# Kernel tuning notes

Measured on AMD Instinct MI355X. Metric: run time of the kernel, lower is better.

The kernel has to match this reference:

```python
import jax, jax.numpy as jnp
import numpy as np

B, CQ, CKV, E = 8, 256, 256, 256
H, W = 64, 64
HP, WP = 32, 32


def setup_inputs() -> dict:
    key = jax.random.key(0)
    ks = jax.random.split(key, 6)
    C = jax.random.normal(ks[0], (B, CQ, H, W), dtype=jnp.float32)
    P = jax.random.normal(ks[1], (B, CKV, HP, WP), dtype=jnp.float32)
    # 1x1 conv weights, kaiming-ish scale; stored as [out_ch, in_ch]
    theta_w = jax.random.normal(ks[2], (E, CQ), dtype=jnp.float32) * (1.0 / np.sqrt(CQ))
    phi_w = jax.random.normal(ks[3], (E, CKV), dtype=jnp.float32) * (1.0 / np.sqrt(CKV))
    g_w = jax.random.normal(ks[4], (E, CKV), dtype=jnp.float32) * (1.0 / np.sqrt(CKV))
    out_w = jax.random.normal(ks[5], (CQ, E), dtype=jnp.float32) * (1.0 / np.sqrt(E))
    return {"C": C, "P": P, "theta_w": theta_w, "phi_w": phi_w, "g_w": g_w, "out_w": out_w}


def reference(C, P, theta_w, phi_w, g_w, out_w):
    b, _, h, w = C.shape
    e = theta_w.shape[0]
    # 1x1 convs are channel GEMMs
    theta_C = jnp.einsum('bchw,ec->behw', C, theta_w).reshape(b, e, h * w)   # [B,E,Nq]
    phi_P = jnp.einsum('bchw,ec->behw', P, phi_w).reshape(b, e, -1)          # [B,E,Nkv]
    g_P = jnp.einsum('bchw,ec->behw', P, g_w).reshape(b, e, -1)              # [B,E,Nkv]
    attn = jnp.einsum('ben,bem->bnm', theta_C, phi_P) / (e ** 0.5)           # [B,Nq,Nkv]
    attn = jax.nn.softmax(attn, axis=-1)
    out = jnp.einsum('bem,bnm->ben', g_P, attn).reshape(b, e, h, w)          # [B,E,H,W]
    out = jnp.einsum('behw,ce->bchw', out, out_w)                            # [B,CQ,H,W]
    return jnp.concatenate([C, out], axis=1)
```

## Files before the change

### kernel.cpp

```cpp
#include <hip/hip_runtime.h>


typedef __attribute__((ext_vector_type(8))) short short8;
typedef __attribute__((ext_vector_type(16))) float f32x16;
typedef unsigned short ushort_t;

__device__ __forceinline__ unsigned short f2bf(float f) {
    unsigned int u = __float_as_uint(f);
    u += 0x7FFFu + ((u >> 16) & 1u);
    return (unsigned short)(u >> 16);
}
__device__ __forceinline__ unsigned int pack2bf(float a, float b) {
    return (unsigned int)f2bf(a) | ((unsigned int)f2bf(b) << 16);
}
__device__ __forceinline__ void gload16(const ushort_t* g, ushort_t* l) {
    __builtin_amdgcn_global_load_lds(
        (const __attribute__((address_space(1))) unsigned int*)g,
        (__attribute__((address_space(3))) unsigned int*)l, 16, 0, 0);
}
__device__ __forceinline__ f32x16 zero16() {
    f32x16 z;
#pragma unroll
    for (int i = 0; i < 16; ++i) z[i] = 0.f;
    return z;
}

__global__ __launch_bounds__(256) void prep_w(const float* __restrict__ thw,
                                              const float* __restrict__ phw,
                                              const float* __restrict__ ow,
                                              const float* __restrict__ gw,
                                              ushort_t* __restrict__ thc,
                                              ushort_t* __restrict__ phc,
                                              ushort_t* __restrict__ w2c) {
    int blk = blockIdx.x;
    int t = threadIdx.x;
    if (blk < 512) {
        int which = blk >> 8;
        int e = blk & 255, c = t;
        const float* src = which ? phw : thw;
        ushort_t* dst = which ? phc : thc;
        int idx = ((((e >> 5) * 16 + (c >> 4)) * 64 + ((c >> 3) & 1) * 32 + (e & 31)) << 3) + (c & 7);
        dst[idx] = f2bf(src[e * 256 + c]);
    } else {
        int c0 = (blk - 512) * 8;
        float acc[8] = {};
        for (int e = 0; e < 256; ++e) {
            float g = gw[e * 256 + t];
#pragma unroll
            for (int i = 0; i < 8; ++i) acc[i] += ow[(c0 + i) * 256 + e] * g;
        }
#pragma unroll
        for (int i = 0; i < 8; ++i) {
            int c = c0 + i, k = t;
            int idx = ((((c >> 5) * 16 + (k >> 4)) * 64 + ((k >> 3) & 1) * 32 + (c & 31)) << 3) + (k & 7);
            w2c[idx] = f2bf(acc[i]);
        }
    }
}

__global__ __launch_bounds__(256, 2) void proj_all(const ushort_t* __restrict__ thc,
                                                   const ushort_t* __restrict__ phc,
                                                   const ushort_t* __restrict__ w2c,
                                                   const float* __restrict__ C,
                                                   const float* __restrict__ P,
                                                   ushort_t* __restrict__ thetaA,
                                                   ushort_t* __restrict__ phiA,
                                                   ushort_t* __restrict__ gVx) {
    __shared__ float Xs[256][68];
    int blk = blockIdx.x;
    int tid = threadIdx.x, lane = tid & 63, wid = tid >> 6;
    int l31 = lane & 31, lh = lane >> 5;
    const int wq = wid & 1, we = wid >> 1;

    int role, b, nt, N;
    const ushort_t* Wc;
    const float* Xg;
    ushort_t* outp;
    float scale = 1.f;
    if (blk < 512) {
        role = 0; b = blk & 7; nt = blk >> 3;
        Wc = thc; Xg = C + (size_t)b * 1048576; outp = thetaA + (size_t)b * 1048576;
        N = 4096; scale = 1.4426950408889634f / 16.0f;
    } else if (blk < 640) {
        int r = blk - 512; role = 1; b = r & 7; nt = r >> 3;
        Wc = phc; Xg = P + (size_t)b * 262144; outp = phiA + (size_t)b * 262144;
        N = 1024;
    } else {
        int r = blk - 640; role = 2; b = r & 7; nt = r >> 3;
        Wc = w2c; Xg = P + (size_t)b * 262144; outp = gVx + (size_t)b * 262144;
        N = 1024;
    }

    {
        const float* Xb = Xg + nt * 64;
#pragma unroll
        for (int i = 0; i < 16; ++i) {
            int idx = i * 256 + tid;
            int row = idx >> 4, c4 = (idx & 15) * 4;
            *(float4*)&Xs[row][c4] = *(const float4*)(Xb + (size_t)row * N + c4);
        }
    }
    __syncthreads();

    const int n0 = nt * 64 + wq * 32;
    const int ncr = (n0 >> 5) * 16;
    const int q = wq * 32 + l31;

    f32x16 o[4];
#pragma unroll
    for (int f = 0; f < 4; ++f) o[f] = zero16();

#pragma unroll
    for (int ks = 0; ks < 16; ++ks) {
        const int cb = ks * 16 + lh * 8;
        union PW { unsigned int u[4]; short8 v; } xw;
#pragma unroll
        for (int j = 0; j < 4; ++j)
            xw.u[j] = pack2bf(Xs[cb + 2 * j][q], Xs[cb + 2 * j + 1][q]);
#pragma unroll
        for (int f2 = 0; f2 < 4; ++f2) {
            int f = we * 4 + f2;
            short8 wf = *(const short8*)(Wc + ((size_t)(f * 16 + ks) * 64 + lane) * 8);
            o[f2] = __builtin_amdgcn_mfma_f32_32x32x16_bf16(wf, xw.v, o[f2], 0, 0, 0);
        }
    }

    if (role < 2) {
#pragma unroll
        for (int f2 = 0; f2 < 4; ++f2) {
            int f = we * 4 + f2;
#pragma unroll
            for (int rq = 0; rq < 4; ++rq) {
                uint2 st;
                st.x = pack2bf(o[f2][4 * rq + 0] * scale, o[f2][4 * rq + 1] * scale);
                st.y = pack2bf(o[f2][4 * rq + 2] * scale, o[f2][4 * rq + 3] * scale);
                size_t addr = ((size_t)(ncr + f * 2 + (rq >> 1)) * 64 + l31 + 32 * (rq & 1)) * 8 + 4 * lh;
                *(uint2*)(outp + addr) = st;
            }
        }
    } else {
        int kvq = (n0 >> 4) + (l31 >> 4);
        int lhw = 32 * ((l31 >> 3) & 1);
        int kl = l31 & 7;
#pragma unroll
        for (int f2 = 0; f2 < 4; ++f2) {
            int f = we * 4 + f2;
#pragma unroll
            for (int r2 = 0; r2 < 16; ++r2) {
                int crow = (r2 & 3) + 8 * (r2 >> 2) + 4 * lh;
                size_t addr = ((size_t)(f * 64 + kvq) * 64 + crow + lhw) * 8 + kl;
                outp[addr] = f2bf(o[f2][r2]);
            }
        }
    }
}

__global__ __launch_bounds__(512, 2) void attn9(const ushort_t* __restrict__ thetaA,
                                                const ushort_t* __restrict__ phiA,
                                                const ushort_t* __restrict__ gVx,
                                                const float* __restrict__ Cf,
                                                float* __restrict__ out) {
    const int b = blockIdx.x & 7, qt = blockIdx.x >> 3;
    const int tid = threadIdx.x, lane = tid & 63, wid = tid >> 6;
    const int l31 = lane & 31, lh = lane >> 5;
    const int g = wid & 3, eh = wid >> 2;

    __shared__ __align__(16) ushort_t smem[65536];

    const ushort_t* thA = thetaA + (size_t)b * 1048576;
    const ushort_t* phA = phiA + (size_t)b * 262144;
    const ushort_t* gVb = gVx + (size_t)b * 262144;

    auto stage = [&](int j, int d) {
        if (wid < 4) {
            const ushort_t* src = phA + (size_t)j * 16384 + (size_t)wid * 4096 + lane * 8;
            ushort_t* dst = smem + d * 16384 + wid * 4096;
#pragma unroll
            for (int i = 0; i < 8; ++i) gload16(src + i * 512, dst + i * 512);
        } else {
            int w = wid - 4;
#pragma unroll
            for (int q2 = 0; q2 < 2; ++q2) {
                int f = w * 2 + q2;
#pragma unroll
                for (int jj = 0; jj < 4; ++jj) {
                    const ushort_t* src = gVb + ((size_t)(f * 64 + j * 4 + jj) * 64 + lane) * 8;
                    ushort_t* dst = smem + 32768 + d * 16384 + f * 2048 + jj * 512;
                    gload16(src, dst);
                }
            }
        }
    };

    stage(0, 0);

    short8 qf[16];
    {
        const int qcr = (qt * 4 + g) * 16;
#pragma unroll
        for (int ks = 0; ks < 16; ++ks)
            qf[ks] = *(const short8*)(thA + ((size_t)(qcr + ks) * 64 + lane) * 8);
    }

    f32x16 o[4];
#pragma unroll
    for (int f = 0; f < 4; ++f) o[f] = zero16();
    float rl = 0.f;

    const size_t cbase = (size_t)b * 1048576 + (size_t)qt * 128 + (size_t)l31 * 4;
    const size_t dofs = (size_t)b * 1048576;
    size_t cpo = 0;
    float4 cpv;

    for (int it = 0; it < 16; ++it) {
        asm volatile("s_waitcnt vmcnt(0)" ::: "memory");
        __builtin_amdgcn_s_barrier();
        __builtin_amdgcn_sched_barrier(0);
        if (it < 15) stage(it + 1, (it + 1) & 1);

        if (it > 0) *(float4*)(out + cpo + dofs) = cpv;
        cpo = cbase + (size_t)(it * 16 + 2 * wid + lh) * 4096;
        cpv = *(const float4*)(Cf + cpo);

        const ushort_t* Kb = smem + (it & 1) * 16384;
        const ushort_t* Vb = smem + 32768 + (it & 1) * 16384 + eh * 8192;

        f32x16 s0 = zero16(), s1 = zero16();
#pragma unroll
        for (int ks = 0; ks < 16; ++ks) {
            short8 kf0 = *(const short8*)(Kb + (size_t)ks * 512 + lane * 8);
            short8 kf1 = *(const short8*)(Kb + 8192 + (size_t)ks * 512 + lane * 8);
            s0 = __builtin_amdgcn_mfma_f32_32x32x16_bf16(kf0, qf[ks], s0, 0, 0, 0);
            s1 = __builtin_amdgcn_mfma_f32_32x32x16_bf16(kf1, qf[ks], s1, 0, 0, 0);
        }

        float ps = 0.f;
#pragma unroll
        for (int r = 0; r < 16; ++r) {
            s0[r] = __builtin_amdgcn_exp2f(s0[r]);
            s1[r] = __builtin_amdgcn_exp2f(s1[r]);
            ps += s0[r] + s1[r];
        }
        ps += __shfl_xor(ps, 32);
        rl += ps;

        unsigned int a0 = pack2bf(s0[0], s0[1]),   b0 = pack2bf(s0[4], s0[5]);
        unsigned int a1 = pack2bf(s0[2], s0[3]),   b1 = pack2bf(s0[6], s0[7]);
        unsigned int a2 = pack2bf(s0[8], s0[9]),   b2 = pack2bf(s0[12], s0[13]);
        unsigned int a3 = pack2bf(s0[10], s0[11]), b3 = pack2bf(s0[14], s0[15]);
        asm volatile("v_permlane32_swap_b32 %0, %1" : "+v"(a0), "+v"(b0));
        asm volatile("v_permlane32_swap_b32 %0, %1" : "+v"(a1), "+v"(b1));
        asm volatile("v_permlane32_swap_b32 %0, %1" : "+v"(a2), "+v"(b2));
        asm volatile("v_permlane32_swap_b32 %0, %1" : "+v"(a3), "+v"(b3));
        unsigned int c0 = pack2bf(s1[0], s1[1]),   d0 = pack2bf(s1[4], s1[5]);
        unsigned int c1 = pack2bf(s1[2], s1[3]),   d1 = pack2bf(s1[6], s1[7]);
        unsigned int c2 = pack2bf(s1[8], s1[9]),   d2 = pack2bf(s1[12], s1[13]);
        unsigned int c3 = pack2bf(s1[10], s1[11]), d3 = pack2bf(s1[14], s1[15]);
        asm volatile("v_permlane32_swap_b32 %0, %1" : "+v"(c0), "+v"(d0));
        asm volatile("v_permlane32_swap_b32 %0, %1" : "+v"(c1), "+v"(d1));
        asm volatile("v_permlane32_swap_b32 %0, %1" : "+v"(c2), "+v"(d2));
        asm volatile("v_permlane32_swap_b32 %0, %1" : "+v"(c3), "+v"(d3));
        union PW { unsigned int u[4]; short8 v; };
        PW pw[4];
        pw[0].u[0] = a0; pw[0].u[1] = a1; pw[0].u[2] = b0; pw[0].u[3] = b1;
        pw[1].u[0] = a2; pw[1].u[1] = a3; pw[1].u[2] = b2; pw[1].u[3] = b3;
        pw[2].u[0] = c0; pw[2].u[1] = c1; pw[2].u[2] = d0; pw[2].u[3] = d1;
        pw[3].u[0] = c2; pw[3].u[1] = c3; pw[3].u[2] = d2; pw[3].u[3] = d3;

        __builtin_amdgcn_s_setprio(1);
#pragma unroll
        for (int ks2 = 0; ks2 < 4; ++ks2) {
            short8 pf = pw[ks2].v;
#pragma unroll
            for (int fl = 0; fl < 4; ++fl) {
                short8 vf = *(const short8*)(Vb + (size_t)fl * 2048 + ks2 * 512 + lane * 8);
                o[fl] = __builtin_amdgcn_mfma_f32_32x32x16_bf16(vf, pf, o[fl], 0, 0, 0);
            }
        }
        __builtin_amdgcn_s_setprio(0);
    }

    *(float4*)(out + cpo + dofs) = cpv;

    float inv = 1.f / rl;
    float* ob = out + (size_t)b * 2097152 + (size_t)256 * 4096 + qt * 128 + g * 32 + l31;
#pragma unroll
    for (int fl = 0; fl < 4; ++fl) {
#pragma unroll
        for (int r = 0; r < 16; ++r) {
            int e = eh * 128 + fl * 32 + (r & 3) + 8 * (r >> 2) + 4 * lh;
            ob[(size_t)e * 4096] = o[fl][r] * inv;
        }
    }
}


extern "C" void kernel_launch(void* const* d_in, const int* in_sizes, int n_in,
                              void* d_out, int out_size, void* d_ws, size_t ws_size,
                              hipStream_t stream) {
    const float* C       = (const float*)d_in[0];
    const float* P       = (const float*)d_in[1];
    const float* theta_w = (const float*)d_in[2];
    const float* phi_w   = (const float*)d_in[3];
    const float* g_w     = (const float*)d_in[4];
    const float* out_w   = (const float*)d_in[5];
    float* out = (float*)d_out;

    ushort_t* ws = (ushort_t*)d_ws;
    ushort_t* thetaA = ws;
    ushort_t* phiA   = ws + 8388608;
    ushort_t* gVx    = ws + 10485760;
    ushort_t* thWc   = ws + 12582912;
    ushort_t* phWc   = ws + 12648448;
    ushort_t* w2c    = ws + 12713984;

    prep_w<<<544, 256, 0, stream>>>(theta_w, phi_w, out_w, g_w, thWc, phWc, w2c);
    proj_all<<<768, 256, 0, stream>>>(thWc, phWc, w2c, C, P, thetaA, phiA, gVx);
    attn9<<<256, 512, 0, stream>>>(thetaA, phiA, gVx, C, out);
}
```

Baseline: 123.3 us.

## Halve attention tile size per block to double grid and occupancy

The attention kernel now handles 64 query positions per block instead of 128, iterating over 32 half-size KV chunks with half the shared memory and fewer accumulators per wave. The grid doubles to 512 blocks and launch bounds allow 4 blocks per CU, which is meant to raise occupancy and balance load across CUs. The C passthrough copy is rescheduled to run every fourth iteration. In exchange, each K/V tile is loaded by twice as many blocks and each block issues twice as many barriers.

```diff
diff --git a/kernel.cpp b/kernel.cpp
--- a/kernel.cpp
+++ b/kernel.cpp
@@ -155,17 +155,17 @@
     }
 }
 
-__global__ __launch_bounds__(512, 2) void attn9(const ushort_t* __restrict__ thetaA,
-                                                const ushort_t* __restrict__ phiA,
-                                                const ushort_t* __restrict__ gVx,
-                                                const float* __restrict__ Cf,
-                                                float* __restrict__ out) {
+__global__ __launch_bounds__(512, 4) void attn10(const ushort_t* __restrict__ thetaA,
+                                                 const ushort_t* __restrict__ phiA,
+                                                 const ushort_t* __restrict__ gVx,
+                                                 const float* __restrict__ Cf,
+                                                 float* __restrict__ out) {
     const int b = blockIdx.x & 7, qt = blockIdx.x >> 3;
     const int tid = threadIdx.x, lane = tid & 63, wid = tid >> 6;
     const int l31 = lane & 31, lh = lane >> 5;
-    const int g = wid & 3, eh = wid >> 2;
-
-    __shared__ __align__(16) ushort_t smem[65536];
+    const int g = wid & 1, eq = wid >> 1;
+
+    __shared__ __align__(16) ushort_t smem[32768];
 
     const ushort_t* thA = thetaA + (size_t)b * 1048576;
     const ushort_t* phA = phiA + (size_t)b * 262144;
@@ -173,20 +173,20 @@
 
     auto stage = [&](int j, int d) {
         if (wid < 4) {
-            const ushort_t* src = phA + (size_t)j * 16384 + (size_t)wid * 4096 + lane * 8;
-            ushort_t* dst = smem + d * 16384 + wid * 4096;
-#pragma unroll
-            for (int i = 0; i < 8; ++i) gload16(src + i * 512, dst + i * 512);
+#pragma unroll
+            for (int i = 0; i < 4; ++i) {
+                const ushort_t* src = phA + ((size_t)j * 16 + wid * 4 + i) * 512 + lane * 8;
+                gload16(src, smem + d * 8192 + (wid * 4 + i) * 512);
+            }
         } else {
             int w = wid - 4;
 #pragma unroll
             for (int q2 = 0; q2 < 2; ++q2) {
                 int f = w * 2 + q2;
 #pragma unroll
-                for (int jj = 0; jj < 4; ++jj) {
-                    const ushort_t* src = gVb + ((size_t)(f * 64 + j * 4 + jj) * 64 + lane) * 8;
-                    ushort_t* dst = smem + 32768 + d * 16384 + f * 2048 + jj * 512;
-                    gload16(src, dst);
+                for (int jj = 0; jj < 2; ++jj) {
+                    const ushort_t* src = gVb + ((size_t)(f * 64 + 2 * j + jj) * 64 + lane) * 8;
+                    gload16(src, smem + 16384 + d * 8192 + f * 1024 + jj * 512);
                 }
             }
         }
@@ -196,50 +196,49 @@
 
     short8 qf[16];
     {
-        const int qcr = (qt * 4 + g) * 16;
+        const int qcr = (qt * 2 + g) * 16;
 #pragma unroll
         for (int ks = 0; ks < 16; ++ks)
             qf[ks] = *(const short8*)(thA + ((size_t)(qcr + ks) * 64 + lane) * 8);
     }
 
-    f32x16 o[4];
-#pragma unroll
-    for (int f = 0; f < 4; ++f) o[f] = zero16();
+    f32x16 o[2];
+    o[0] = zero16(); o[1] = zero16();
     float rl = 0.f;
 
-    const size_t cbase = (size_t)b * 1048576 + (size_t)qt * 128 + (size_t)l31 * 4;
-    const size_t dofs = (size_t)b * 1048576;
+    const float* Cb = Cf + (size_t)b * 1048576 + (size_t)qt * 64;
+    float* outCb = out + (size_t)b * 2097152 + (size_t)qt * 64;
     size_t cpo = 0;
     float4 cpv;
 
-    for (int it = 0; it < 16; ++it) {
+    for (int it = 0; it < 32; ++it) {
         asm volatile("s_waitcnt vmcnt(0)" ::: "memory");
         __builtin_amdgcn_s_barrier();
         __builtin_amdgcn_sched_barrier(0);
-        if (it < 15) stage(it + 1, (it + 1) & 1);
-
-        if (it > 0) *(float4*)(out + cpo + dofs) = cpv;
-        cpo = cbase + (size_t)(it * 16 + 2 * wid + lh) * 4096;
-        cpv = *(const float4*)(Cf + cpo);
-
-        const ushort_t* Kb = smem + (it & 1) * 16384;
-        const ushort_t* Vb = smem + 32768 + (it & 1) * 16384 + eh * 8192;
-
-        f32x16 s0 = zero16(), s1 = zero16();
+        if (it < 31) stage(it + 1, (it + 1) & 1);
+
+        if ((it & 3) == 0) {
+            if (it > 0) *(float4*)(outCb + cpo) = cpv;
+            int idx = (it >> 2) * 512 + tid;
+            cpo = (size_t)(idx >> 4) * 4096 + (idx & 15) * 4;
+            cpv = *(const float4*)(Cb + cpo);
+        }
+
+        const ushort_t* Kb = smem + (it & 1) * 8192;
+        const ushort_t* Vb = smem + 16384 + (it & 1) * 8192 + eq * 2048;
+
+        f32x16 s0 = zero16();
 #pragma unroll
         for (int ks = 0; ks < 16; ++ks) {
-            short8 kf0 = *(const short8*)(Kb + (size_t)ks * 512 + lane * 8);
-            short8 kf1 = *(const short8*)(Kb + 8192 + (size_t)ks * 512 + lane * 8);
-            s0 = __builtin_amdgcn_mfma_f32_32x32x16_bf16(kf0, qf[ks], s0, 0, 0, 0);
-            s1 = __builtin_amdgcn_mfma_f32_32x32x16_bf16(kf1, qf[ks], s1, 0, 0, 0);
+            short8 kf = *(const short8*)(Kb + (size_t)ks * 512 + lane * 8);
+            s0 = __builtin_amdgcn_mfma_f32_32x32x16_bf16(kf, qf[ks], s0, 0, 0, 0);
         }
 
         float ps = 0.f;
 #pragma unroll
         for (int r = 0; r < 16; ++r) {
             s0[r] = __builtin_amdgcn_exp2f(s0[r]);
-            s1[r] = __builtin_amdgcn_exp2f(s1[r]);
-            ps += s0[r] + s1[r];
+            ps += s0[r];
         }
         ps += __shfl_xor(ps, 32);
         rl += ps;
@@ -252,43 +251,33 @@
         asm volatile("v_permlane32_swap_b32 %0, %1" : "+v"(a1), "+v"(b1));
         asm volatile("v_permlane32_swap_b32 %0, %1" : "+v"(a2), "+v"(b2));
         asm volatile("v_permlane32_swap_b32 %0, %1" : "+v"(a3), "+v"(b3));
-        unsigned int c0 = pack2bf(s1[0], s1[1]),   d0 = pack2bf(s1[4], s1[5]);
-        unsigned int c1 = pack2bf(s1[2], s1[3]),   d1 = pack2bf(s1[6], s1[7]);
-        unsigned int c2 = pack2bf(s1[8], s1[9]),   d2 = pack2bf(s1[12], s1[13]);
-        unsigned int c3 = pack2bf(s1[10], s1[11]), d3 = pack2bf(s1[14], s1[15]);
-        asm volatile("v_permlane32_swap_b32 %0, %1" : "+v"(c0), "+v"(d0));
-        asm volatile("v_permlane32_swap_b32 %0, %1" : "+v"(c1), "+v"(d1));
-        asm volatile("v_permlane32_swap_b32 %0, %1" : "+v"(c2), "+v"(d2));
-        asm volatile("v_permlane32_swap_b32 %0, %1" : "+v"(c3), "+v"(d3));
         union PW { unsigned int u[4]; short8 v; };
-        PW pw[4];
-        pw[0].u[0] = a0; pw[0].u[1] = a1; pw[0].u[2] = b0; pw[0].u[3] = b1;
-        pw[1].u[0] = a2; pw[1].u[1] = a3; pw[1].u[2] = b2; pw[1].u[3] = b3;
-        pw[2].u[0] = c0; pw[2].u[1] = c1; pw[2].u[2] = d0; pw[2].u[3] = d1;
-        pw[3].u[0] = c2; pw[3].u[1] = c3; pw[3].u[2] = d2; pw[3].u[3] = d3;
+        PW pw0, pw1;
+        pw0.u[0] = a0; pw0.u[1] = a1; pw0.u[2] = b0; pw0.u[3] = b1;
+        pw1.u[0] = a2; pw1.u[1] = a3; pw1.u[2] = b2; pw1.u[3] = b3;
 
         __builtin_amdgcn_s_setprio(1);
 #pragma unroll
-        for (int ks2 = 0; ks2 < 4; ++ks2) {
-            short8 pf = pw[ks2].v;
-#pragma unroll
-            for (int fl = 0; fl < 4; ++fl) {
-                short8 vf = *(const short8*)(Vb + (size_t)fl * 2048 + ks2 * 512 + lane * 8);
+        for (int ks2 = 0; ks2 < 2; ++ks2) {
+            short8 pf = ks2 ? pw1.v : pw0.v;
+#pragma unroll
+            for (int fl = 0; fl < 2; ++fl) {
+                short8 vf = *(const short8*)(Vb + (size_t)fl * 1024 + ks2 * 512 + lane * 8);
                 o[fl] = __builtin_amdgcn_mfma_f32_32x32x16_bf16(vf, pf, o[fl], 0, 0, 0);
             }
         }
         __builtin_amdgcn_s_setprio(0);
     }
 
-    *(float4*)(out + cpo + dofs) = cpv;
+    *(float4*)(outCb + cpo) = cpv;
 
     float inv = 1.f / rl;
-    float* ob = out + (size_t)b * 2097152 + (size_t)256 * 4096 + qt * 128 + g * 32 + l31;
-#pragma unroll
-    for (int fl = 0; fl < 4; ++fl) {
+    float* ob = out + (size_t)b * 2097152 + (size_t)256 * 4096 + qt * 64 + g * 32 + l31;
+#pragma unroll
+    for (int fl = 0; fl < 2; ++fl) {
 #pragma unroll
         for (int r = 0; r < 16; ++r) {
-            int e = eh * 128 + fl * 32 + (r & 3) + 8 * (r >> 2) + 4 * lh;
+            int e = eq * 64 + fl * 32 + (r & 3) + 8 * (r >> 2) + 4 * lh;
             ob[(size_t)e * 4096] = o[fl][r] * inv;
         }
     }
@@ -316,5 +305,5 @@
 
     prep_w<<<544, 256, 0, stream>>>(theta_w, phi_w, out_w, g_w, thWc, phWc, w2c);
     proj_all<<<768, 256, 0, stream>>>(thWc, phWc, w2c, C, P, thetaA, phiA, gVx);
-    attn9<<<256, 512, 0, stream>>>(thetaA, phiA, gVx, C, out);
-}
+    attn10<<<512, 512, 0, stream>>>(thetaA, phiA, gVx, C, out);
+}
```

Result: slower. 173.3 us (+40.6%).

## Split QK^T across wave pairs and share P tiles through LDS

Applied to the files above, without the earlier changes.

Before, two waves sharing a query group each computed the full 32x64 score tile, so QK^T work and exp were done twice. Now each wave computes half of the KV columns and writes its bf16 probabilities to a new LDS buffer. A barrier follows, then both waves read all four P fragments for the PV MFMAs, and row sums are combined through shared memory at the end. This removes the redundant score MFMAs and exponentials, at the cost of an extra block-wide barrier per iteration, LDS traffic for P, and more shared memory use that may lower occupancy.

```diff
diff --git a/kernel.cpp b/kernel.cpp
--- a/kernel.cpp
+++ b/kernel.cpp
@@ -155,17 +155,19 @@
     }
 }
 
-__global__ __launch_bounds__(512, 2) void attn9(const ushort_t* __restrict__ thetaA,
-                                                const ushort_t* __restrict__ phiA,
-                                                const ushort_t* __restrict__ gVx,
-                                                const float* __restrict__ Cf,
-                                                float* __restrict__ out) {
+__global__ __launch_bounds__(512, 2) void attn11(const ushort_t* __restrict__ thetaA,
+                                                 const ushort_t* __restrict__ phiA,
+                                                 const ushort_t* __restrict__ gVx,
+                                                 const float* __restrict__ Cf,
+                                                 float* __restrict__ out) {
     const int b = blockIdx.x & 7, qt = blockIdx.x >> 3;
     const int tid = threadIdx.x, lane = tid & 63, wid = tid >> 6;
     const int l31 = lane & 31, lh = lane >> 5;
-    const int g = wid & 3, eh = wid >> 2;
+    const int qg = wid & 3, z = wid >> 2;
 
     __shared__ __align__(16) ushort_t smem[65536];
+    __shared__ __align__(16) ushort_t Pl[8192];
+    __shared__ float rlS[2][4][32];
 
     const ushort_t* thA = thetaA + (size_t)b * 1048576;
     const ushort_t* phA = phiA + (size_t)b * 262144;
@@ -196,7 +198,7 @@
 
     short8 qf[16];
     {
-        const int qcr = (qt * 4 + g) * 16;
+        const int qcr = (qt * 4 + qg) * 16;
 #pragma unroll
         for (int ks = 0; ks < 16; ++ks)
             qf[ks] = *(const short8*)(thA + ((size_t)(qcr + ks) * 64 + lane) * 8);
@@ -222,58 +224,53 @@
         cpo = cbase + (size_t)(it * 16 + 2 * wid + lh) * 4096;
         cpv = *(const float4*)(Cf + cpo);
 
-        const ushort_t* Kb = smem + (it & 1) * 16384;
-        const ushort_t* Vb = smem + 32768 + (it & 1) * 16384 + eh * 8192;
-
-        f32x16 s0 = zero16(), s1 = zero16();
+        const ushort_t* Kb = smem + (it & 1) * 16384 + z * 8192;
+        const ushort_t* Vb = smem + 32768 + (it & 1) * 16384 + z * 8192;
+
+        f32x16 s = zero16();
+        __builtin_amdgcn_s_setprio(1);
 #pragma unroll
         for (int ks = 0; ks < 16; ++ks) {
-            short8 kf0 = *(const short8*)(Kb + (size_t)ks * 512 + lane * 8);
-            short8 kf1 = *(const short8*)(Kb + 8192 + (size_t)ks * 512 + lane * 8);
-            s0 = __builtin_amdgcn_mfma_f32_32x32x16_bf16(kf0, qf[ks], s0, 0, 0, 0);
-            s1 = __builtin_amdgcn_mfma_f32_32x32x16_bf16(kf1, qf[ks], s1, 0, 0, 0);
-        }
-
-        float ps = 0.f;
-#pragma unroll
-        for (int r = 0; r < 16; ++r) {
-            s0[r] = __builtin_amdgcn_exp2f(s0[r]);
-            s1[r] = __builtin_amdgcn_exp2f(s1[r]);
-            ps += s0[r] + s1[r];
-        }
+            short8 kf = *(const short8*)(Kb + (size_t)ks * 512 + lane * 8);
+            s = __builtin_amdgcn_mfma_f32_32x32x16_bf16(kf, qf[ks], s, 0, 0, 0);
+        }
+        __builtin_amdgcn_s_setprio(0);
+
+#pragma unroll
+        for (int r = 0; r < 16; ++r) s[r] = __builtin_amdgcn_exp2f(s[r]);
+        float t0 = (s[0] + s[1]) + (s[2] + s[3]);
+        float t1 = (s[4] + s[5]) + (s[6] + s[7]);
+        float t2 = (s[8] + s[9]) + (s[10] + s[11]);
+        float t3 = (s[12] + s[13]) + (s[14] + s[15]);
+        float ps = (t0 + t1) + (t2 + t3);
         ps += __shfl_xor(ps, 32);
         rl += ps;
 
-        unsigned int a0 = pack2bf(s0[0], s0[1]),   b0 = pack2bf(s0[4], s0[5]);
-        unsigned int a1 = pack2bf(s0[2], s0[3]),   b1 = pack2bf(s0[6], s0[7]);
-        unsigned int a2 = pack2bf(s0[8], s0[9]),   b2 = pack2bf(s0[12], s0[13]);
-        unsigned int a3 = pack2bf(s0[10], s0[11]), b3 = pack2bf(s0[14], s0[15]);
+        unsigned int a0 = pack2bf(s[0], s[1]),   b0 = pack2bf(s[4], s[5]);
+        unsigned int a1 = pack2bf(s[2], s[3]),   b1 = pack2bf(s[6], s[7]);
+        unsigned int a2 = pack2bf(s[8], s[9]),   b2 = pack2bf(s[12], s[13]);
+        unsigned int a3 = pack2bf(s[10], s[11]), b3 = pack2bf(s[14], s[15]);
         asm volatile("v_permlane32_swap_b32 %0, %1" : "+v"(a0), "+v"(b0));
         asm volatile("v_permlane32_swap_b32 %0, %1" : "+v"(a1), "+v"(b1));
         asm volatile("v_permlane32_swap_b32 %0, %1" : "+v"(a2), "+v"(b2));
         asm volatile("v_permlane32_swap_b32 %0, %1" : "+v"(a3), "+v"(b3));
-        unsigned int c0 = pack2bf(s1[0], s1[1]),   d0 = pack2bf(s1[4], s1[5]);
-        unsigned int c1 = pack2bf(s1[2], s1[3]),   d1 = pack2bf(s1[6], s1[7]);
-        unsigned int c2 = pack2bf(s1[8], s1[9]),   d2 = pack2bf(s1[12], s1[13]);
-        unsigned int c3 = pack2bf(s1[10], s1[11]), d3 = pack2bf(s1[14], s1[15]);
-        asm volatile("v_permlane32_swap_b32 %0, %1" : "+v"(c0), "+v"(d0));
-        asm volatile("v_permlane32_swap_b32 %0, %1" : "+v"(c1), "+v"(d1));
-        asm volatile("v_permlane32_swap_b32 %0, %1" : "+v"(c2), "+v"(d2));
-        asm volatile("v_permlane32_swap_b32 %0, %1" : "+v"(c3), "+v"(d3));
         union PW { unsigned int u[4]; short8 v; };
-        PW pw[4];
-        pw[0].u[0] = a0; pw[0].u[1] = a1; pw[0].u[2] = b0; pw[0].u[3] = b1;
-        pw[1].u[0] = a2; pw[1].u[1] = a3; pw[1].u[2] = b2; pw[1].u[3] = b3;
-        pw[2].u[0] = c0; pw[2].u[1] = c1; pw[2].u[2] = d0; pw[2].u[3] = d1;
-        pw[3].u[0] = c2; pw[3].u[1] = c3; pw[3].u[2] = d2; pw[3].u[3] = d3;
+        PW pw0, pw1;
+        pw0.u[0] = a0; pw0.u[1] = a1; pw0.u[2] = b0; pw0.u[3] = b1;
+        pw1.u[0] = a2; pw1.u[1] = a3; pw1.u[2] = b2; pw1.u[3] = b3;
+
+        *(short8*)(Pl + ((size_t)(qg * 4 + 2 * z + 0) * 64 + lane) * 8) = pw0.v;
+        *(short8*)(Pl + ((size_t)(qg * 4 + 2 * z + 1) * 64 + lane) * 8) = pw1.v;
+        asm volatile("s_waitcnt lgkmcnt(0)" ::: "memory");
+        __builtin_amdgcn_s_barrier();
 
         __builtin_amdgcn_s_setprio(1);
 #pragma unroll
-        for (int ks2 = 0; ks2 < 4; ++ks2) {
-            short8 pf = pw[ks2].v;
+        for (int j = 0; j < 4; ++j) {
+            short8 pf = *(const short8*)(Pl + ((size_t)(qg * 4 + j) * 64 + lane) * 8);
 #pragma unroll
             for (int fl = 0; fl < 4; ++fl) {
-                short8 vf = *(const short8*)(Vb + (size_t)fl * 2048 + ks2 * 512 + lane * 8);
+                short8 vf = *(const short8*)(Vb + (size_t)fl * 2048 + j * 512 + lane * 8);
                 o[fl] = __builtin_amdgcn_mfma_f32_32x32x16_bf16(vf, pf, o[fl], 0, 0, 0);
             }
         }
@@ -282,13 +279,15 @@
 
     *(float4*)(out + cpo + dofs) = cpv;
 
-    float inv = 1.f / rl;
-    float* ob = out + (size_t)b * 2097152 + (size_t)256 * 4096 + qt * 128 + g * 32 + l31;
+    if (lane < 32) rlS[z][qg][l31] = rl;
+    __syncthreads();
+    float inv = 1.f / (rlS[0][qg][l31] + rlS[1][qg][l31]);
+    float* ob = out + (size_t)b * 2097152 + (size_t)256 * 4096 + qt * 128 + qg * 32 + l31;
 #pragma unroll
     for (int fl = 0; fl < 4; ++fl) {
 #pragma unroll
         for (int r = 0; r < 16; ++r) {
-            int e = eh * 128 + fl * 32 + (r & 3) + 8 * (r >> 2) + 4 * lh;
+            int e = z * 128 + fl * 32 + (r & 3) + 8 * (r >> 2) + 4 * lh;
             ob[(size_t)e * 4096] = o[fl][r] * inv;
         }
     }
@@ -316,5 +315,5 @@
 
     prep_w<<<544, 256, 0, stream>>>(theta_w, phi_w, out_w, g_w, thWc, phWc, w2c);
     proj_all<<<768, 256, 0, stream>>>(thWc, phWc, w2c, C, P, thetaA, phiA, gVx);
-    attn9<<<256, 512, 0, stream>>>(thetaA, phiA, gVx, C, out);
-}
+    attn11<<<256, 512, 0, stream>>>(thetaA, phiA, gVx, C, out);
+}
```

Result: faster. 113.4 us (-8.0%).
